# Optimization experiments

Measured on AMD Instinct MI355X. Metric: run time of the kernel, lower is better.

Reference implementation:

```python
import jax, jax.numpy as jnp
import numpy as np

NUM_WIRES = 20
DEPTH = 4


def setup_inputs() -> dict:
    key = jax.random.key(0)
    x = jax.random.normal(key, (NUM_WIRES,), dtype=jnp.float32)
    return {"x": x}


def _apply_1q(state, gate, wire):
    # state: flat [2^n] complex; apply 2x2 gate on `wire`
    s = state.reshape(2 ** wire, 2, -1)
    return jnp.einsum('ab,ibj->iaj', gate, s).reshape(-1)


def _apply_cnot(state, control):
    # CNOT on adjacent wires (control, control+1): flip target where control==1
    s = state.reshape(2 ** control, 2, 2, -1)
    s = jnp.concatenate([s[:, :1], s[:, 1:, ::-1]], axis=1)
    return s.reshape(-1)


def _simulate(x):
    n = NUM_WIRES
    state = jnp.zeros(2 ** n, dtype=jnp.complex64).at[0].set(1.0)
    half = (x.astype(jnp.float32) * 0.5)
    c = jnp.cos(half).astype(jnp.complex64)  # [n]
    s = jnp.sin(half).astype(jnp.complex64)  # [n]
    for _ in range(DEPTH):
        for w in range(n):
            cw, sw = c[w], s[w]
            rx = jnp.stack([jnp.stack([cw, -1j * sw]), jnp.stack([-1j * sw, cw])])
            ry = jnp.stack([jnp.stack([cw, -sw]), jnp.stack([sw, cw])])
            state = _apply_1q(state, rx, w)
            state = _apply_1q(state, ry, w)
        for w in range(n - 1):
            state = _apply_cnot(state, w)
    probs = jnp.abs(state) ** 2  # real float32 [2^n]
    expz = []
    for i in range(n):
        p = probs.reshape(2 ** i, 2, -1).sum(axis=(0, 2))
        expz.append(p[0] - p[1])
    return jnp.stack(expz).astype(jnp.float32)  # [n] <Z_i>


def reference(x):
    return _simulate(x)
```

## Files before the change

### kernel.cpp

```cpp
#include <hip/hip_runtime.h>


#define NW 20

__device__ __forceinline__ float2 cmul(float2 a, float2 b) {
    return make_float2(a.x*b.x - a.y*b.y, a.x*b.y + a.y*b.x);
}

__device__ __forceinline__ void apply_gate(float2& a0, float2& a1,
                                           float2 u00, float2 u01,
                                           float2 u10, float2 u11) {
    float2 b0, b1;
    b0.x = u00.x*a0.x - u00.y*a0.y + u01.x*a1.x - u01.y*a1.y;
    b0.y = u00.x*a0.y + u00.y*a0.x + u01.x*a1.y + u01.y*a1.x;
    b1.x = u10.x*a0.x - u10.y*a0.y + u11.x*a1.x - u11.y*a1.y;
    b1.y = u10.x*a0.y + u10.y*a0.x + u11.x*a1.y + u11.y*a1.x;
    a0 = b0; a1 = b1;
}

__device__ __forceinline__ float2 shflx(float2 v, int m) {
    float2 r;
    r.x = __shfl_xor(v.x, m, 64);
    r.y = __shfl_xor(v.y, m, 64);
    return r;
}

__device__ __forceinline__ unsigned sfx(unsigned x) {
    x ^= x >> 1; x ^= x >> 2; x ^= x >> 4; x ^= x >> 8; x ^= x >> 16; return x;
}

template<int A>
__device__ __forceinline__ void gate_regbit4(float2 (&amp)[4], const float2* Gw) {
    float2 u00 = Gw[0], u01 = Gw[1], u10 = Gw[2], u11 = Gw[3];
    #pragma unroll
    for (int r = 0; r < 4; r++)
        if (!(r & (1 << A)))
            apply_gate(amp[r], amp[r | (1 << A)], u00, u01, u10, u11);
}

template<int A, int LM>
__device__ __forceinline__ void swap_reg_lane4(float2 (&amp)[4], unsigned lane) {
    bool hb = (lane & (unsigned)LM) != 0u;
    #pragma unroll
    for (int r = 0; r < 4; r++) {
        if (!(r & (1 << A))) {
            float2 lo = amp[r], hi = amp[r | (1 << A)];
            float2 xs = hb ? lo : hi;
            float2 ys = shflx(xs, LM);
            amp[r]            = hb ? ys : lo;
            amp[r | (1 << A)] = hb ? hi : ys;
        }
    }
}

__device__ __forceinline__ void prep_Gs(const float* __restrict__ x, float2* Gs,
                                        unsigned t) {
    if (t < NW) {
        float h = 0.5f * x[t];
        float c = cosf(h), s = sinf(h);
        float cc = c*c, ss = s*s, cs = c*s;
        Gs[t*4+0] = make_float2(cc,  ss);
        Gs[t*4+1] = make_float2(-cs, -cs);
        Gs[t*4+2] = make_float2(cs,  -cs);
        Gs[t*4+3] = make_float2(cc,  -ss);
    }
}

template<int MODE>
__global__ __launch_bounds__(1024) void stageA(const float* __restrict__ x,
                                               const float2* __restrict__ src,
                                               float2* __restrict__ dst) {
    __shared__ float2 lds[4096];
    __shared__ float2 Gs[4*NW];
    const unsigned t = threadIdx.x;
    prep_Gs(x, Gs, t);
    __syncthreads();
    const unsigned lane = t & 63u, wv = t >> 6;
    const unsigned w0 = wv & 1u, w1 = (wv >> 1) & 1u, w2 = (wv >> 2) & 1u, w3 = wv >> 3;
    const unsigned H   = blockIdx.x;
    const unsigned Hp  = H ^ (H >> 1);
    const unsigned inj = (H & 1u) << 11;
    const unsigned lb  = (wv << 8) | (lane << 2);
    const unsigned gb  = (lb ^ (lb >> 1)) ^ inj;

    float2 amp[4];
    if (MODE == 1) {
        const float4* q = (const float4*)(src + ((size_t)Hp << 12) + (gb & ~3u));
        float4 q0 = q[0], q1 = q[1];
        float2 e0 = make_float2(q0.x,q0.y), e1 = make_float2(q0.z,q0.w);
        float2 e2 = make_float2(q1.x,q1.y), e3 = make_float2(q1.z,q1.w);
        bool s2 = (gb & 2u) != 0u;
        amp[0] = s2 ? e2 : e0;
        amp[1] = s2 ? e3 : e1;
        amp[2] = s2 ? e1 : e3;
        amp[3] = s2 ? e0 : e2;
    } else {
        float2 P = make_float2(1.0f, 0.0f);
        #pragma unroll
        for (int b = 12; b <= 19; b++)
            P = cmul(P, Gs[(19-b)*4 + (int)((Hp >> (b-12)) & 1u)*2]);
        #pragma unroll
        for (int b = 2; b <= 11; b++)
            P = cmul(P, Gs[(19-b)*4 + (int)((gb >> b) & 1u)*2]);
        float2 T[4];
        #pragma unroll
        for (int j = 0; j < 4; j++)
            T[j] = cmul(P, cmul(Gs[19*4 + (j&1)*2], Gs[18*4 + ((j>>1)&1)*2]));
        bool s2 = (gb & 2u) != 0u;
        amp[0] = s2 ? T[2] : T[0];
        amp[1] = s2 ? T[3] : T[1];
        amp[2] = s2 ? T[1] : T[3];
        amp[3] = s2 ? T[0] : T[2];
    }

    gate_regbit4<0>(amp, Gs + 19*4);
    gate_regbit4<1>(amp, Gs + 18*4);
    swap_reg_lane4<0,1>(amp, lane);
    swap_reg_lane4<1,2>(amp, lane);
    gate_regbit4<0>(amp, Gs + 17*4);
    gate_regbit4<1>(amp, Gs + 16*4);
    swap_reg_lane4<0,4>(amp, lane);
    swap_reg_lane4<1,8>(amp, lane);
    gate_regbit4<0>(amp, Gs + 15*4);
    gate_regbit4<1>(amp, Gs + 14*4);
    swap_reg_lane4<0,16>(amp, lane);
    swap_reg_lane4<1,32>(amp, lane);
    gate_regbit4<0>(amp, Gs + 13*4);
    gate_regbit4<1>(amp, Gs + 12*4);
    #pragma unroll
    for (int k = 0; k < 4; k++) lds[lane | ((unsigned)k << 6) | (wv << 8)] = amp[k];
    __syncthreads();
    #pragma unroll
    for (int k = 0; k < 4; k++)
        amp[k] = lds[lane | (w0 << 6) | (w1 << 7) | ((unsigned)k << 8) | (w2 << 10) | (w3 << 11)];
    gate_regbit4<0>(amp, Gs + 11*4);
    gate_regbit4<1>(amp, Gs + 10*4);
    __syncthreads();
    #pragma unroll
    for (int k = 0; k < 4; k++) lds[lane | ((unsigned)k << 6) | (wv << 8)] = amp[k];
    __syncthreads();
    #pragma unroll
    for (int k = 0; k < 4; k++)
        amp[k] = lds[lane | (w2 << 6) | (w3 << 7) | (w0 << 8) | (w1 << 9) | ((unsigned)k << 10)];
    gate_regbit4<0>(amp, Gs + 9*4);
    gate_regbit4<1>(amp, Gs + 8*4);
    float2* d = dst + ((size_t)H << 12);
    #pragma unroll
    for (int k = 0; k < 4; k++)
        d[lane | (w0 << 6) | (w1 << 7) | (w2 << 8) | (w3 << 9) | ((unsigned)k << 10)] = amp[k];
}

template<int FUSE>
__global__ __launch_bounds__(1024) void stageB(const float* __restrict__ x,
                                               float2* __restrict__ st,
                                               float* __restrict__ partial) {
    __shared__ float2 lds[4096];
    __shared__ float2 Gs[4*NW];
    const unsigned t = threadIdx.x;
    prep_Gs(x, Gs, t);
    __syncthreads();
    const unsigned lane = t & 63u, wv = t >> 6;
    const unsigned w0 = wv & 1u, w1 = (wv >> 1) & 1u, w2 = (wv >> 2) & 1u, w3 = wv >> 3;
    const unsigned bb = blockIdx.x;
    const unsigned m = lane & 15u, l4 = (lane >> 4) & 1u, l5 = lane >> 5;

    float2 amp[4];
    #pragma unroll
    for (int k = 0; k < 4; k++) {
        unsigned h = (unsigned)k | (l4 << 2) | (l5 << 3) | (wv << 4);
        amp[k] = st[((size_t)h << 12) | (bb << 4) | m];
    }
    gate_regbit4<0>(amp, Gs + 7*4);
    gate_regbit4<1>(amp, Gs + 6*4);
    swap_reg_lane4<0,16>(amp, lane);
    swap_reg_lane4<1,32>(amp, lane);
    gate_regbit4<0>(amp, Gs + 5*4);
    gate_regbit4<1>(amp, Gs + 4*4);
    #pragma unroll
    for (int k = 0; k < 4; k++) lds[lane | ((unsigned)k << 6) | (wv << 8)] = amp[k];
    __syncthreads();
    #pragma unroll
    for (int k = 0; k < 4; k++)
        amp[k] = lds[lane | (w0 << 6) | (w1 << 7) | ((unsigned)k << 8) | (w2 << 10) | (w3 << 11)];
    gate_regbit4<0>(amp, Gs + 3*4);
    gate_regbit4<1>(amp, Gs + 2*4);
    __syncthreads();
    #pragma unroll
    for (int k = 0; k < 4; k++) lds[lane | ((unsigned)k << 6) | (wv << 8)] = amp[k];
    __syncthreads();
    #pragma unroll
    for (int k = 0; k < 4; k++)
        amp[k] = lds[lane | (w2 << 6) | (w3 << 7) | (w0 << 8) | (w1 << 9) | ((unsigned)k << 10)];
    gate_regbit4<0>(amp, Gs + 1*4);
    gate_regbit4<1>(amp, Gs + 0*4);

    if (!FUSE) {
        #pragma unroll
        for (int k = 0; k < 4; k++) {
            unsigned h = l4 | (l5 << 1) | (w0 << 2) | (w1 << 3) | (w2 << 4) | (w3 << 5)
                       | (((unsigned)k & 1u) << 6) | (((unsigned)k >> 1) << 7);
            st[((size_t)h << 12) | (bb << 4) | m] = amp[k];
        }
    } else {
        float p[4];
        #pragma unroll
        for (int k = 0; k < 4; k++) p[k] = amp[k].x*amp[k].x + amp[k].y*amp[k].y;
        float S19 = (p[0] + p[1]) - (p[2] + p[3]);
        float D   = p[0] - p[1] - p[2] + p[3];
        unsigned v = m | (bb << 4) | (l4 << 12) | (l5 << 13) | (w0 << 14)
                   | (w1 << 15) | (w2 << 16) | (w3 << 17);
        unsigned cm = sfx(v);
        float acc[NW];
        acc[0] = S19; acc[1] = D;
        #pragma unroll
        for (int w = 2; w < NW; w++)
            acc[w] = ((cm >> (19 - w)) & 1u) ? -D : D;

        __syncthreads();
        float* red = (float*)lds;
        #pragma unroll
        for (int w = 0; w < NW; w++) {
            float s = acc[w];
            #pragma unroll
            for (int off = 32; off; off >>= 1) s += __shfl_down(s, off, 64);
            if (lane == 0) red[wv*NW + w] = s;
        }
        __syncthreads();
        if (t < NW) {
            float s = 0.0f;
            #pragma unroll
            for (int v16 = 0; v16 < 16; v16++) s += red[v16*NW + (int)t];
            partial[bb*NW + t] = s;
        }
    }
}

__global__ __launch_bounds__(256) void reduce_out(const float* __restrict__ partial,
                                                  float* __restrict__ out) {
    __shared__ float red[4*NW];
    unsigned t = threadIdx.x;
    float vals[NW];
    #pragma unroll
    for (int w = 0; w < NW; w++) vals[w] = partial[t*NW + w];
    #pragma unroll
    for (int w = 0; w < NW; w++) {
        float v = vals[w];
        #pragma unroll
        for (int off = 32; off; off >>= 1) v += __shfl_down(v, off, 64);
        if ((t & 63u) == 0u) red[(t >> 6)*NW + w] = v;
    }
    __syncthreads();
    if (t < NW) out[t] = red[t] + red[NW+t] + red[2*NW+t] + red[3*NW+t];
}

extern "C" void kernel_launch(void* const* d_in, const int* in_sizes, int n_in,
                              void* d_out, int out_size, void* d_ws, size_t ws_size,
                              hipStream_t stream) {
    (void)in_sizes; (void)n_in; (void)out_size; (void)ws_size;
    const float* x = (const float*)d_in[0];
    float* out = (float*)d_out;

    char* ws = (char*)d_ws;
    float*  partial = (float*)(ws + 1024);
    float2* buf0    = (float2*)(ws + 65536);
    float2* buf1    = (float2*)(ws + 65536 + (size_t)(8u << 20));

    stageA<0><<<256, 1024, 0, stream>>>(x, buf1 , buf0);
    stageB<0><<<256, 1024, 0, stream>>>(x, buf0, nullptr);
    stageA<1><<<256, 1024, 0, stream>>>(x, buf0, buf1);
    stageB<0><<<256, 1024, 0, stream>>>(x, buf1, nullptr);
    stageA<1><<<256, 1024, 0, stream>>>(x, buf1, buf0);
    stageB<1><<<256, 1024, 0, stream>>>(x, buf0, partial);
    reduce_out<<<1, 256, 0, stream>>>(partial, out);
}
```

Baseline: 63.68 us.

## Fuse layer passes into four kernels with CNOT-parity masked gates

```diff
diff --git a/kernel.cpp b/kernel.cpp
--- a/kernel.cpp
+++ b/kernel.cpp
@@ -25,12 +25,12 @@
     return r;
 }
 
-__device__ __forceinline__ unsigned sfx(unsigned x) {
-    x ^= x >> 1; x ^= x >> 2; x ^= x >> 4; x ^= x >> 8; x ^= x >> 16; return x;
+__device__ __forceinline__ unsigned pfx2(unsigned x) {
+    x ^= x >> 2; x ^= x >> 4; x ^= x >> 8; x ^= x >> 16; return x;
 }
 
 template<int A>
-__device__ __forceinline__ void gate_regbit4(float2 (&amp)[4], const float2* Gw) {
+__device__ __forceinline__ void gate_regbit(float2 (&amp)[4], const float2* Gw) {
     float2 u00 = Gw[0], u01 = Gw[1], u10 = Gw[2], u11 = Gw[3];
     #pragma unroll
     for (int r = 0; r < 4; r++)
@@ -50,6 +50,20 @@
             amp[r]            = hb ? ys : lo;
             amp[r | (1 << A)] = hb ? hi : ys;
         }
+    }
+}
+
+template<int M, int SEL, int RH>
+__device__ __forceinline__ void gate_mreg(float2 (&amp)[4], const float2* Gw,
+                                          unsigned Rk) {
+    float2 u00 = Gw[0], u01 = Gw[1], u10 = Gw[2], u11 = Gw[3];
+    #pragma unroll
+    for (int r = 0; r < 4; r++) {
+        if (r & SEL) continue;
+        int rp = r ^ M;
+        unsigned fl = (Rk + (unsigned)__popc((unsigned)r & (unsigned)RH)) & 1u;
+        if (fl == 0u) apply_gate(amp[r], amp[rp], u00, u01, u10, u11);
+        else          apply_gate(amp[rp], amp[r], u00, u01, u10, u11);
     }
 }
 
@@ -66,9 +80,58 @@
     }
 }
 
-template<int MODE>
-__global__ __launch_bounds__(1024) void stageA(const float* __restrict__ x,
-                                               const float2* __restrict__ src,
+__device__ __forceinline__ void masked_high(float2 (&amp)[4], float2* lds,
+                                            const float2* Gs, unsigned lane,
+                                            unsigned wv) {
+    const unsigned w0 = wv & 1u, w1 = (wv >> 1) & 1u, w2 = (wv >> 2) & 1u, w3 = wv >> 3;
+    const unsigned l3 = (lane >> 3) & 1u, l4 = (lane >> 4) & 1u, l5 = lane >> 5;
+    const unsigned wpar = w0 ^ w1 ^ w2 ^ w3;
+    gate_mreg<3,2,0>(amp, Gs + 0*4, 0u);
+    #pragma unroll
+    for (int k = 0; k < 4; k++) lds[lane | ((unsigned)k << 6) | (wv << 8)] = amp[k];
+    __syncthreads();
+    #pragma unroll
+    for (int k = 0; k < 4; k++)
+        amp[k] = lds[lane | ((unsigned)(k>>1) << 6) | (w3 << 7) | (w0 << 8)
+                     | (w1 << 9) | (w2 << 10) | ((unsigned)(k&1) << 11)];
+    __syncthreads();
+    gate_mreg<3,2,0>(amp, Gs + 1*4, w3);
+    #pragma unroll
+    for (int k = 0; k < 4; k++) lds[lane | ((unsigned)k << 6) | (wv << 8)] = amp[k];
+    __syncthreads();
+    #pragma unroll
+    for (int k = 0; k < 4; k++)
+        amp[k] = lds[lane | ((unsigned)(k>>1) << 6) | (w2 << 7) | (w0 << 8)
+                     | (w1 << 9) | ((unsigned)(k&1) << 10) | (w3 << 11)];
+    __syncthreads();
+    gate_mreg<3,2,0>(amp, Gs + 2*4, w2 ^ w3);
+    #pragma unroll
+    for (int k = 0; k < 4; k++) lds[lane | ((unsigned)k << 6) | (wv << 8)] = amp[k];
+    __syncthreads();
+    #pragma unroll
+    for (int k = 0; k < 4; k++)
+        amp[k] = lds[lane | ((unsigned)(k>>1) << 6) | (w1 << 7) | (w0 << 8)
+                     | ((unsigned)(k&1) << 9) | (w2 << 10) | (w3 << 11)];
+    __syncthreads();
+    gate_mreg<3,2,0>(amp, Gs + 3*4, w1 ^ w2 ^ w3);
+    #pragma unroll
+    for (int k = 0; k < 4; k++) lds[lane | ((unsigned)k << 6) | (wv << 8)] = amp[k];
+    __syncthreads();
+    #pragma unroll
+    for (int k = 0; k < 4; k++)
+        amp[k] = lds[lane | ((unsigned)(k>>1) << 6) | (w0 << 7) | ((unsigned)(k&1) << 8)
+                     | (w1 << 9) | (w2 << 10) | (w3 << 11)];
+    __syncthreads();
+    gate_mreg<3,2,0>(amp, Gs + 4*4, wpar);
+    swap_reg_lane4<1,16>(amp, lane);
+    gate_mreg<3,1,0>(amp, Gs + 5*4, l4 ^ wpar);
+    swap_reg_lane4<0,8>(amp, lane);
+    gate_mreg<3,2,0>(amp, Gs + 6*4, l3 ^ l4 ^ wpar);
+    swap_reg_lane4<1,32>(amp, lane);
+    gate_mreg<3,1,0>(amp, Gs + 7*4, l5 ^ l3 ^ l4 ^ wpar);
+}
+
+__global__ __launch_bounds__(1024) void passA1(const float* __restrict__ x,
                                                float2* __restrict__ dst) {
     __shared__ float2 lds[4096];
     __shared__ float2 Gs[4*NW];
@@ -84,9 +147,139 @@
     const unsigned gb  = (lb ^ (lb >> 1)) ^ inj;
 
     float2 amp[4];
-    if (MODE == 1) {
+    {
+        float2 P = make_float2(1.0f, 0.0f);
+        #pragma unroll
+        for (int b = 12; b <= 19; b++)
+            P = cmul(P, Gs[(19-b)*4 + (int)((Hp >> (b-12)) & 1u)*2]);
+        #pragma unroll
+        for (int b = 2; b <= 11; b++)
+            P = cmul(P, Gs[(19-b)*4 + (int)((gb >> b) & 1u)*2]);
+        float2 T[4];
+        #pragma unroll
+        for (int j = 0; j < 4; j++)
+            T[j] = cmul(P, cmul(Gs[19*4 + (j&1)*2], Gs[18*4 + ((j>>1)&1)*2]));
+        bool s2 = (gb & 2u) != 0u;
+        amp[0] = s2 ? T[2] : T[0];
+        amp[1] = s2 ? T[3] : T[1];
+        amp[2] = s2 ? T[1] : T[3];
+        amp[3] = s2 ? T[0] : T[2];
+    }
+    gate_regbit<0>(amp, Gs + 19*4);
+    gate_regbit<1>(amp, Gs + 18*4);
+    swap_reg_lane4<0,1>(amp, lane);
+    swap_reg_lane4<1,2>(amp, lane);
+    gate_regbit<0>(amp, Gs + 17*4);
+    gate_regbit<1>(amp, Gs + 16*4);
+    swap_reg_lane4<0,4>(amp, lane);
+    swap_reg_lane4<1,8>(amp, lane);
+    gate_regbit<0>(amp, Gs + 15*4);
+    gate_regbit<1>(amp, Gs + 14*4);
+    swap_reg_lane4<0,16>(amp, lane);
+    swap_reg_lane4<1,32>(amp, lane);
+    gate_regbit<0>(amp, Gs + 13*4);
+    gate_regbit<1>(amp, Gs + 12*4);
+    #pragma unroll
+    for (int k = 0; k < 4; k++) lds[lane | ((unsigned)k << 6) | (wv << 8)] = amp[k];
+    __syncthreads();
+    #pragma unroll
+    for (int k = 0; k < 4; k++)
+        amp[k] = lds[lane | (w0 << 6) | (w1 << 7) | ((unsigned)k << 8) | (w2 << 10) | (w3 << 11)];
+    gate_regbit<0>(amp, Gs + 11*4);
+    gate_regbit<1>(amp, Gs + 10*4);
+    __syncthreads();
+    #pragma unroll
+    for (int k = 0; k < 4; k++) lds[lane | ((unsigned)k << 6) | (wv << 8)] = amp[k];
+    __syncthreads();
+    #pragma unroll
+    for (int k = 0; k < 4; k++)
+        amp[k] = lds[lane | (w2 << 6) | (w3 << 7) | (w0 << 8) | (w1 << 9) | ((unsigned)k << 10)];
+    gate_regbit<0>(amp, Gs + 9*4);
+    gate_regbit<1>(amp, Gs + 8*4);
+    float2* d = dst + ((size_t)H << 12);
+    #pragma unroll
+    for (int k = 0; k < 4; k++)
+        d[lane | (w0 << 6) | (w1 << 7) | (w2 << 8) | (w3 << 9) | ((unsigned)k << 10)] = amp[k];
+}
+
+__global__ __launch_bounds__(1024) void passB2(const float* __restrict__ x,
+                                               float2* __restrict__ st) {
+    __shared__ float2 lds[4096];
+    __shared__ float2 Gs[4*NW];
+    const unsigned t = threadIdx.x, lane = t & 63u, wv = t >> 6;
+    const unsigned w0 = wv & 1u, w1 = (wv >> 1) & 1u, w2 = (wv >> 2) & 1u, w3 = wv >> 3;
+    const unsigned bb = blockIdx.x;
+    const unsigned l012 = lane & 7u;
+    const unsigned l3 = (lane >> 3) & 1u, l4 = (lane >> 4) & 1u, l5 = lane >> 5;
+
+    float2 amp[4];
+    const unsigned base = l012 | (bb << 3) | (l5 << 11) | (l3 << 14) | (l4 << 15)
+                        | (w0 << 16) | (w1 << 17) | (w2 << 18) | (w3 << 19);
+    #pragma unroll
+    for (int k = 0; k < 4; k++)
+        amp[k] = st[base | ((unsigned)(k & 1) << 12) | ((unsigned)(k >> 1) << 13)];
+    prep_Gs(x, Gs, t);
+    __syncthreads();
+
+    gate_regbit<0>(amp, Gs + 7*4);
+    gate_regbit<1>(amp, Gs + 6*4);
+    swap_reg_lane4<0,8>(amp, lane);
+    gate_regbit<0>(amp, Gs + 5*4);
+    swap_reg_lane4<1,16>(amp, lane);
+    gate_regbit<1>(amp, Gs + 4*4);
+    #pragma unroll
+    for (int k = 0; k < 4; k++) lds[lane | ((unsigned)k << 6) | (wv << 8)] = amp[k];
+    __syncthreads();
+    #pragma unroll
+    for (int k = 0; k < 4; k++)
+        amp[k] = lds[lane | (w0 << 6) | (w1 << 7) | ((unsigned)(k&1) << 8)
+                     | ((unsigned)(k>>1) << 9) | (w2 << 10) | (w3 << 11)];
+    __syncthreads();
+    gate_regbit<0>(amp, Gs + 3*4);
+    gate_regbit<1>(amp, Gs + 2*4);
+    #pragma unroll
+    for (int k = 0; k < 4; k++) lds[lane | ((unsigned)k << 6) | (wv << 8)] = amp[k];
+    __syncthreads();
+    #pragma unroll
+    for (int k = 0; k < 4; k++)
+        amp[k] = lds[lane | (w2 << 6) | (w3 << 7) | (w0 << 8) | (w1 << 9)
+                     | ((unsigned)(k&1) << 10) | ((unsigned)(k>>1) << 11)];
+    __syncthreads();
+    gate_regbit<0>(amp, Gs + 1*4);
+    gate_regbit<1>(amp, Gs + 0*4);
+
+    masked_high(amp, lds, Gs, lane, wv);
+
+    const unsigned sb = l012 | (bb << 3) | (l5 << 13) | (l3 << 14) | (l4 << 15)
+                      | (w0 << 16) | (w1 << 17) | (w2 << 18) | (w3 << 19);
+    #pragma unroll
+    for (int k = 0; k < 4; k++)
+        st[sb | ((unsigned)(k >> 1) << 11) | ((unsigned)(k & 1) << 12)] = amp[k];
+}
+
+__global__ __launch_bounds__(1024) void passA3(const float* __restrict__ x,
+                                               const float2* __restrict__ src,
+                                               float2* __restrict__ dst) {
+    __shared__ float2 lds[4096];
+    __shared__ float2 Gs[4*NW];
+    const unsigned t = threadIdx.x, lane = t & 63u, wv = t >> 6;
+    const unsigned w0 = wv & 1u, w1 = (wv >> 1) & 1u, w2 = (wv >> 2) & 1u, w3 = wv >> 3;
+    const unsigned H   = blockIdx.x;
+    const unsigned Hp  = H ^ (H >> 1);
+    const unsigned inj = (H & 1u) << 11;
+    const unsigned lb  = (wv << 8) | (lane << 2);
+    const unsigned gb  = (lb ^ (lb >> 1)) ^ inj;
+
+    float4 q0, q1;
+    {
         const float4* q = (const float4*)(src + ((size_t)Hp << 12) + (gb & ~3u));
-        float4 q0 = q[0], q1 = q[1];
+        q0 = q[0]; q1 = q[1];
+    }
+    prep_Gs(x, Gs, t);
+    __syncthreads();
+
+    float2 amp[4];
+    {
         float2 e0 = make_float2(q0.x,q0.y), e1 = make_float2(q0.z,q0.w);
         float2 e2 = make_float2(q1.x,q1.y), e3 = make_float2(q1.z,q1.w);
         bool s2 = (gb & 2u) != 0u;
@@ -94,47 +287,29 @@
         amp[1] = s2 ? e3 : e1;
         amp[2] = s2 ? e1 : e3;
         amp[3] = s2 ? e0 : e2;
-    } else {
-        float2 P = make_float2(1.0f, 0.0f);
-        #pragma unroll
-        for (int b = 12; b <= 19; b++)
-            P = cmul(P, Gs[(19-b)*4 + (int)((Hp >> (b-12)) & 1u)*2]);
-        #pragma unroll
-        for (int b = 2; b <= 11; b++)
-            P = cmul(P, Gs[(19-b)*4 + (int)((gb >> b) & 1u)*2]);
-        float2 T[4];
-        #pragma unroll
-        for (int j = 0; j < 4; j++)
-            T[j] = cmul(P, cmul(Gs[19*4 + (j&1)*2], Gs[18*4 + ((j>>1)&1)*2]));
-        bool s2 = (gb & 2u) != 0u;
-        amp[0] = s2 ? T[2] : T[0];
-        amp[1] = s2 ? T[3] : T[1];
-        amp[2] = s2 ? T[1] : T[3];
-        amp[3] = s2 ? T[0] : T[2];
-    }
-
-    gate_regbit4<0>(amp, Gs + 19*4);
-    gate_regbit4<1>(amp, Gs + 18*4);
+    }
+    gate_regbit<0>(amp, Gs + 19*4);
+    gate_regbit<1>(amp, Gs + 18*4);
     swap_reg_lane4<0,1>(amp, lane);
     swap_reg_lane4<1,2>(amp, lane);
-    gate_regbit4<0>(amp, Gs + 17*4);
-    gate_regbit4<1>(amp, Gs + 16*4);
+    gate_regbit<0>(amp, Gs + 17*4);
+    gate_regbit<1>(amp, Gs + 16*4);
     swap_reg_lane4<0,4>(amp, lane);
     swap_reg_lane4<1,8>(amp, lane);
-    gate_regbit4<0>(amp, Gs + 15*4);
-    gate_regbit4<1>(amp, Gs + 14*4);
+    gate_regbit<0>(amp, Gs + 15*4);
+    gate_regbit<1>(amp, Gs + 14*4);
     swap_reg_lane4<0,16>(amp, lane);
     swap_reg_lane4<1,32>(amp, lane);
-    gate_regbit4<0>(amp, Gs + 13*4);
-    gate_regbit4<1>(amp, Gs + 12*4);
+    gate_regbit<0>(amp, Gs + 13*4);
+    gate_regbit<1>(amp, Gs + 12*4);
     #pragma unroll
     for (int k = 0; k < 4; k++) lds[lane | ((unsigned)k << 6) | (wv << 8)] = amp[k];
     __syncthreads();
     #pragma unroll
     for (int k = 0; k < 4; k++)
         amp[k] = lds[lane | (w0 << 6) | (w1 << 7) | ((unsigned)k << 8) | (w2 << 10) | (w3 << 11)];
-    gate_regbit4<0>(amp, Gs + 11*4);
-    gate_regbit4<1>(amp, Gs + 10*4);
+    gate_regbit<0>(amp, Gs + 11*4);
+    gate_regbit<1>(amp, Gs + 10*4);
     __syncthreads();
     #pragma unroll
     for (int k = 0; k < 4; k++) lds[lane | ((unsigned)k << 6) | (wv << 8)] = amp[k];
@@ -142,96 +317,128 @@
     #pragma unroll
     for (int k = 0; k < 4; k++)
         amp[k] = lds[lane | (w2 << 6) | (w3 << 7) | (w0 << 8) | (w1 << 9) | ((unsigned)k << 10)];
-    gate_regbit4<0>(amp, Gs + 9*4);
-    gate_regbit4<1>(amp, Gs + 8*4);
+    gate_regbit<0>(amp, Gs + 9*4);
+    gate_regbit<1>(amp, Gs + 8*4);
+    __syncthreads();
+
+    const unsigned PH = (unsigned)__popc(H) & 1u;
+    const unsigned wpar = w0 ^ w1 ^ w2 ^ w3;
+    const unsigned lpar = (unsigned)__popc(lane) & 1u;
+    const unsigned l0v = lane & 1u, l1v = (lane >> 1) & 1u;
+    const unsigned l3v = (lane >> 3) & 1u, l4v = (lane >> 4) & 1u, l5v = lane >> 5;
+    swap_reg_lane4<0,1>(amp, lane);
+    swap_reg_lane4<1,2>(amp, lane);
+    gate_mreg<1,1,2>(amp, Gs + 19*4, lpar ^ wpar ^ PH);
+    gate_mreg<3,2,0>(amp, Gs + 18*4, lpar ^ wpar ^ PH);
+    swap_reg_lane4<0,4>(amp, lane);
+    gate_mreg<3,1,0>(amp, Gs + 17*4, l3v^l4v^l5v ^ l0v^l1v ^ wpar ^ PH);
+    swap_reg_lane4<1,8>(amp, lane);
+    gate_mreg<3,2,0>(amp, Gs + 16*4, l4v^l5v ^ l0v^l1v ^ wpar ^ PH);
+    swap_reg_lane4<0,16>(amp, lane);
+    gate_mreg<3,1,0>(amp, Gs + 15*4, l5v ^ l0v^l1v ^ wpar ^ PH);
+    swap_reg_lane4<1,32>(amp, lane);
+    gate_mreg<3,2,0>(amp, Gs + 14*4, l0v^l1v ^ wpar ^ PH);
+    #pragma unroll
+    for (int k = 0; k < 4; k++) lds[lane | ((unsigned)k << 6) | (wv << 8)] = amp[k];
+    __syncthreads();
+    #pragma unroll
+    for (int k = 0; k < 4; k++)
+        amp[k] = lds[lane | (w0 << 6) | ((unsigned)(k&1) << 7) | ((unsigned)(k>>1) << 8)
+                     | (w1 << 9) | (w2 << 10) | (w3 << 11)];
+    __syncthreads();
+    gate_mreg<3,2,0>(amp, Gs + 13*4, w1^w2^w3 ^ l0v^l1v ^ PH);
+    #pragma unroll
+    for (int k = 0; k < 4; k++) lds[lane | ((unsigned)k << 6) | (wv << 8)] = amp[k];
+    __syncthreads();
+    #pragma unroll
+    for (int k = 0; k < 4; k++)
+        amp[k] = lds[lane | (w1 << 6) | ((unsigned)(k&1) << 7) | (w0 << 8)
+                     | ((unsigned)(k>>1) << 9) | (w2 << 10) | (w3 << 11)];
+    __syncthreads();
+    gate_mreg<3,2,0>(amp, Gs + 12*4, w2^w3 ^ l0v^l1v ^ PH);
+    #pragma unroll
+    for (int k = 0; k < 4; k++) lds[lane | ((unsigned)k << 6) | (wv << 8)] = amp[k];
+    __syncthreads();
+    #pragma unroll
+    for (int k = 0; k < 4; k++)
+        amp[k] = lds[lane | (w2 << 6) | ((unsigned)(k&1) << 7) | (w0 << 8)
+                     | (w1 << 9) | ((unsigned)(k>>1) << 10) | (w3 << 11)];
+    __syncthreads();
+    gate_mreg<3,2,0>(amp, Gs + 11*4, w3 ^ l0v^l1v ^ PH);
+    #pragma unroll
+    for (int k = 0; k < 4; k++) lds[lane | ((unsigned)k << 6) | (wv << 8)] = amp[k];
+    __syncthreads();
+    #pragma unroll
+    for (int k = 0; k < 4; k++)
+        amp[k] = lds[lane | (w3 << 6) | ((unsigned)(k&1) << 7) | (w0 << 8)
+                     | (w1 << 9) | (w2 << 10) | ((unsigned)(k>>1) << 11)];
+    gate_mreg<3,2,0>(amp, Gs + 10*4, l0v^l1v ^ PH);
+    swap_reg_lane4<0,1>(amp, lane);
+    gate_mreg<3,1,0>(amp, Gs + 9*4, l1v ^ PH);
+    swap_reg_lane4<1,2>(amp, lane);
+    gate_mreg<3,2,0>(amp, Gs + 8*4, PH);
+    const unsigned sb = ((lane >> 2) & 1u) | (l3v << 1) | (l4v << 2) | (l5v << 3)
+                      | (w0 << 4) | (w1 << 5) | (w2 << 6) | (w3 << 7)
+                      | (l0v << 8) | (l1v << 9);
     float2* d = dst + ((size_t)H << 12);
     #pragma unroll
     for (int k = 0; k < 4; k++)
-        d[lane | (w0 << 6) | (w1 << 7) | (w2 << 8) | (w3 << 9) | ((unsigned)k << 10)] = amp[k];
-}
-
-template<int FUSE>
-__global__ __launch_bounds__(1024) void stageB(const float* __restrict__ x,
-                                               float2* __restrict__ st,
+        d[sb | ((unsigned)(k & 1) << 10) | ((unsigned)(k >> 1) << 11)] = amp[k];
+}
+
+__global__ __launch_bounds__(1024) void passB4(const float* __restrict__ x,
+                                               const float2* __restrict__ st,
                                                float* __restrict__ partial) {
     __shared__ float2 lds[4096];
     __shared__ float2 Gs[4*NW];
-    const unsigned t = threadIdx.x;
-    prep_Gs(x, Gs, t);
-    __syncthreads();
-    const unsigned lane = t & 63u, wv = t >> 6;
+    const unsigned t = threadIdx.x, lane = t & 63u, wv = t >> 6;
     const unsigned w0 = wv & 1u, w1 = (wv >> 1) & 1u, w2 = (wv >> 2) & 1u, w3 = wv >> 3;
     const unsigned bb = blockIdx.x;
-    const unsigned m = lane & 15u, l4 = (lane >> 4) & 1u, l5 = lane >> 5;
+    const unsigned l012 = lane & 7u;
+    const unsigned l3 = (lane >> 3) & 1u, l4 = (lane >> 4) & 1u, l5 = lane >> 5;
 
     float2 amp[4];
-    #pragma unroll
-    for (int k = 0; k < 4; k++) {
-        unsigned h = (unsigned)k | (l4 << 2) | (l5 << 3) | (wv << 4);
-        amp[k] = st[((size_t)h << 12) | (bb << 4) | m];
-    }
-    gate_regbit4<0>(amp, Gs + 7*4);
-    gate_regbit4<1>(amp, Gs + 6*4);
-    swap_reg_lane4<0,16>(amp, lane);
-    swap_reg_lane4<1,32>(amp, lane);
-    gate_regbit4<0>(amp, Gs + 5*4);
-    gate_regbit4<1>(amp, Gs + 4*4);
-    #pragma unroll
-    for (int k = 0; k < 4; k++) lds[lane | ((unsigned)k << 6) | (wv << 8)] = amp[k];
-    __syncthreads();
-    #pragma unroll
-    for (int k = 0; k < 4; k++)
-        amp[k] = lds[lane | (w0 << 6) | (w1 << 7) | ((unsigned)k << 8) | (w2 << 10) | (w3 << 11)];
-    gate_regbit4<0>(amp, Gs + 3*4);
-    gate_regbit4<1>(amp, Gs + 2*4);
-    __syncthreads();
-    #pragma unroll
-    for (int k = 0; k < 4; k++) lds[lane | ((unsigned)k << 6) | (wv << 8)] = amp[k];
-    __syncthreads();
-    #pragma unroll
-    for (int k = 0; k < 4; k++)
-        amp[k] = lds[lane | (w2 << 6) | (w3 << 7) | (w0 << 8) | (w1 << 9) | ((unsigned)k << 10)];
-    gate_regbit4<0>(amp, Gs + 1*4);
-    gate_regbit4<1>(amp, Gs + 0*4);
-
-    if (!FUSE) {
-        #pragma unroll
-        for (int k = 0; k < 4; k++) {
-            unsigned h = l4 | (l5 << 1) | (w0 << 2) | (w1 << 3) | (w2 << 4) | (w3 << 5)
-                       | (((unsigned)k & 1u) << 6) | (((unsigned)k >> 1) << 7);
-            st[((size_t)h << 12) | (bb << 4) | m] = amp[k];
-        }
-    } else {
-        float p[4];
-        #pragma unroll
-        for (int k = 0; k < 4; k++) p[k] = amp[k].x*amp[k].x + amp[k].y*amp[k].y;
-        float S19 = (p[0] + p[1]) - (p[2] + p[3]);
-        float D   = p[0] - p[1] - p[2] + p[3];
-        unsigned v = m | (bb << 4) | (l4 << 12) | (l5 << 13) | (w0 << 14)
-                   | (w1 << 15) | (w2 << 16) | (w3 << 17);
-        unsigned cm = sfx(v);
-        float acc[NW];
-        acc[0] = S19; acc[1] = D;
-        #pragma unroll
-        for (int w = 2; w < NW; w++)
-            acc[w] = ((cm >> (19 - w)) & 1u) ? -D : D;
-
-        __syncthreads();
-        float* red = (float*)lds;
-        #pragma unroll
-        for (int w = 0; w < NW; w++) {
-            float s = acc[w];
-            #pragma unroll
-            for (int off = 32; off; off >>= 1) s += __shfl_down(s, off, 64);
-            if (lane == 0) red[wv*NW + w] = s;
-        }
-        __syncthreads();
-        if (t < NW) {
-            float s = 0.0f;
-            #pragma unroll
-            for (int v16 = 0; v16 < 16; v16++) s += red[v16*NW + (int)t];
-            partial[bb*NW + t] = s;
-        }
+    const unsigned base = l012 | (bb << 3) | (l5 << 11) | (l3 << 12) | (l4 << 13)
+                        | (w0 << 14) | (w1 << 15) | (w2 << 16) | (w3 << 17);
+    #pragma unroll
+    for (int k = 0; k < 4; k++)
+        amp[k] = st[base | ((unsigned)(k & 1) << 18) | ((unsigned)(k >> 1) << 19)];
+    prep_Gs(x, Gs, t);
+    __syncthreads();
+
+    masked_high(amp, lds, Gs, lane, wv);
+
+    float p[4];
+    #pragma unroll
+    for (int k = 0; k < 4; k++) p[k] = amp[k].x*amp[k].x + amp[k].y*amp[k].y;
+    const float T = p[0] + p[1] + p[2] + p[3];
+    const float E = (p[0] + p[2]) - (p[1] + p[3]);
+    const float O = (p[0] + p[1]) - (p[2] + p[3]);
+    const unsigned zbase = l012 | (bb << 3) | (l5 << 13) | (l3 << 14) | (l4 << 15)
+                         | (w0 << 16) | (w1 << 17) | (w2 << 18) | (w3 << 19);
+    const unsigned t2 = pfx2(zbase);
+    float acc[NW];
+    #pragma unroll
+    for (int w = 0; w < NW; w++) {
+        int b = 19 - w;
+        float v = (b >= 13) ? T : ((b & 1) ? O : E);
+        acc[w] = ((t2 >> b) & 1u) ? -v : v;
+    }
+    __syncthreads();
+    float* red = (float*)lds;
+    #pragma unroll
+    for (int w = 0; w < NW; w++) {
+        float s = acc[w];
+        #pragma unroll
+        for (int off = 32; off; off >>= 1) s += __shfl_down(s, off, 64);
+        if (lane == 0) red[wv*NW + w] = s;
+    }
+    __syncthreads();
+    if (t < NW) {
+        float s = 0.0f;
+        #pragma unroll
+        for (int v16 = 0; v16 < 16; v16++) s += red[v16*NW + (int)t];
+        partial[bb*NW + t] = s;
     }
 }
 
@@ -265,11 +472,9 @@
     float2* buf0    = (float2*)(ws + 65536);
     float2* buf1    = (float2*)(ws + 65536 + (size_t)(8u << 20));
 
-    stageA<0><<<256, 1024, 0, stream>>>(x, buf1 , buf0);
-    stageB<0><<<256, 1024, 0, stream>>>(x, buf0, nullptr);
-    stageA<1><<<256, 1024, 0, stream>>>(x, buf0, buf1);
-    stageB<0><<<256, 1024, 0, stream>>>(x, buf1, nullptr);
-    stageA<1><<<256, 1024, 0, stream>>>(x, buf1, buf0);
-    stageB<1><<<256, 1024, 0, stream>>>(x, buf0, partial);
+    passA1<<<256, 1024, 0, stream>>>(x, buf0);
+    passB2<<<256, 1024, 0, stream>>>(x, buf0);
+    passA3<<<256, 1024, 0, stream>>>(x, buf0, buf1);
+    passB4<<<256, 1024, 0, stream>>>(x, buf1, partial);
     reduce_out<<<1, 256, 0, stream>>>(partial, out);
 }
```

New measurement: 80.10 us. 1.26x slower.

## Replace second LDS transpose with lane shuffles and prefetch state before gate prep

Applied to the files above, without the earlier changes.

```diff
diff --git a/kernel.cpp b/kernel.cpp
--- a/kernel.cpp
+++ b/kernel.cpp
@@ -30,7 +30,7 @@
 }
 
 template<int A>
-__device__ __forceinline__ void gate_regbit4(float2 (&amp)[4], const float2* Gw) {
+__device__ __forceinline__ void gate_regbit(float2 (&amp)[4], const float2* Gw) {
     float2 u00 = Gw[0], u01 = Gw[1], u10 = Gw[2], u11 = Gw[3];
     #pragma unroll
     for (int r = 0; r < 4; r++)
@@ -73,20 +73,25 @@
     __shared__ float2 lds[4096];
     __shared__ float2 Gs[4*NW];
     const unsigned t = threadIdx.x;
-    prep_Gs(x, Gs, t);
-    __syncthreads();
     const unsigned lane = t & 63u, wv = t >> 6;
     const unsigned w0 = wv & 1u, w1 = (wv >> 1) & 1u, w2 = (wv >> 2) & 1u, w3 = wv >> 3;
+    const unsigned l4v = (lane >> 4) & 1u, l5v = lane >> 5;
     const unsigned H   = blockIdx.x;
     const unsigned Hp  = H ^ (H >> 1);
     const unsigned inj = (H & 1u) << 11;
     const unsigned lb  = (wv << 8) | (lane << 2);
     const unsigned gb  = (lb ^ (lb >> 1)) ^ inj;
 
+    float4 q0, q1;
+    if (MODE == 1) {
+        const float4* q = (const float4*)(src + ((size_t)Hp << 12) + (gb & ~3u));
+        q0 = q[0]; q1 = q[1];
+    }
+    prep_Gs(x, Gs, t);
+    __syncthreads();
+
     float2 amp[4];
     if (MODE == 1) {
-        const float4* q = (const float4*)(src + ((size_t)Hp << 12) + (gb & ~3u));
-        float4 q0 = q[0], q1 = q[1];
         float2 e0 = make_float2(q0.x,q0.y), e1 = make_float2(q0.z,q0.w);
         float2 e2 = make_float2(q1.x,q1.y), e3 = make_float2(q1.z,q1.w);
         bool s2 = (gb & 2u) != 0u;
@@ -113,41 +118,40 @@
         amp[3] = s2 ? T[0] : T[2];
     }
 
-    gate_regbit4<0>(amp, Gs + 19*4);
-    gate_regbit4<1>(amp, Gs + 18*4);
+    gate_regbit<0>(amp, Gs + 19*4);
+    gate_regbit<1>(amp, Gs + 18*4);
     swap_reg_lane4<0,1>(amp, lane);
     swap_reg_lane4<1,2>(amp, lane);
-    gate_regbit4<0>(amp, Gs + 17*4);
-    gate_regbit4<1>(amp, Gs + 16*4);
+    gate_regbit<0>(amp, Gs + 17*4);
+    gate_regbit<1>(amp, Gs + 16*4);
     swap_reg_lane4<0,4>(amp, lane);
     swap_reg_lane4<1,8>(amp, lane);
-    gate_regbit4<0>(amp, Gs + 15*4);
-    gate_regbit4<1>(amp, Gs + 14*4);
-    swap_reg_lane4<0,16>(amp, lane);
-    swap_reg_lane4<1,32>(amp, lane);
-    gate_regbit4<0>(amp, Gs + 13*4);
-    gate_regbit4<1>(amp, Gs + 12*4);
+    gate_regbit<0>(amp, Gs + 15*4);
+    gate_regbit<1>(amp, Gs + 14*4);
+    swap_reg_lane4<0,16>(amp, lane);
+    swap_reg_lane4<1,32>(amp, lane);
+    gate_regbit<0>(amp, Gs + 13*4);
+    gate_regbit<1>(amp, Gs + 12*4);
     #pragma unroll
     for (int k = 0; k < 4; k++) lds[lane | ((unsigned)k << 6) | (wv << 8)] = amp[k];
     __syncthreads();
     #pragma unroll
     for (int k = 0; k < 4; k++)
-        amp[k] = lds[lane | (w0 << 6) | (w1 << 7) | ((unsigned)k << 8) | (w2 << 10) | (w3 << 11)];
-    gate_regbit4<0>(amp, Gs + 11*4);
-    gate_regbit4<1>(amp, Gs + 10*4);
-    __syncthreads();
-    #pragma unroll
-    for (int k = 0; k < 4; k++) lds[lane | ((unsigned)k << 6) | (wv << 8)] = amp[k];
-    __syncthreads();
-    #pragma unroll
-    for (int k = 0; k < 4; k++)
-        amp[k] = lds[lane | (w2 << 6) | (w3 << 7) | (w0 << 8) | (w1 << 9) | ((unsigned)k << 10)];
-    gate_regbit4<0>(amp, Gs + 9*4);
-    gate_regbit4<1>(amp, Gs + 8*4);
+        amp[k] = lds[(lane & 15u) | (w0 << 4) | (w1 << 5) | (w2 << 6) | (w3 << 7)
+                     | ((unsigned)(k & 1) << 8) | ((unsigned)(k >> 1) << 9)
+                     | (l4v << 10) | (l5v << 11)];
+    gate_regbit<0>(amp, Gs + 11*4);
+    gate_regbit<1>(amp, Gs + 10*4);
+    swap_reg_lane4<0,16>(amp, lane);
+    gate_regbit<0>(amp, Gs + 9*4);
+    swap_reg_lane4<1,32>(amp, lane);
+    gate_regbit<1>(amp, Gs + 8*4);
     float2* d = dst + ((size_t)H << 12);
     #pragma unroll
     for (int k = 0; k < 4; k++)
-        d[lane | (w0 << 6) | (w1 << 7) | (w2 << 8) | (w3 << 9) | ((unsigned)k << 10)] = amp[k];
+        d[(lane & 15u) | (w0 << 4) | (w1 << 5) | (w2 << 6) | (w3 << 7)
+          | (l4v << 8) | (l5v << 9)
+          | ((unsigned)(k & 1) << 10) | ((unsigned)(k >> 1) << 11)] = amp[k];
 }
 
 template<int FUSE>
@@ -157,58 +161,55 @@
     __shared__ float2 lds[4096];
     __shared__ float2 Gs[4*NW];
     const unsigned t = threadIdx.x;
-    prep_Gs(x, Gs, t);
-    __syncthreads();
     const unsigned lane = t & 63u, wv = t >> 6;
     const unsigned w0 = wv & 1u, w1 = (wv >> 1) & 1u, w2 = (wv >> 2) & 1u, w3 = wv >> 3;
+    const unsigned m = lane & 15u, l4v = (lane >> 4) & 1u, l5v = lane >> 5;
     const unsigned bb = blockIdx.x;
-    const unsigned m = lane & 15u, l4 = (lane >> 4) & 1u, l5 = lane >> 5;
 
     float2 amp[4];
-    #pragma unroll
-    for (int k = 0; k < 4; k++) {
-        unsigned h = (unsigned)k | (l4 << 2) | (l5 << 3) | (wv << 4);
-        amp[k] = st[((size_t)h << 12) | (bb << 4) | m];
-    }
-    gate_regbit4<0>(amp, Gs + 7*4);
-    gate_regbit4<1>(amp, Gs + 6*4);
-    swap_reg_lane4<0,16>(amp, lane);
-    swap_reg_lane4<1,32>(amp, lane);
-    gate_regbit4<0>(amp, Gs + 5*4);
-    gate_regbit4<1>(amp, Gs + 4*4);
+    const unsigned lbase = m | (bb << 4) | (l4v << 14) | (l5v << 15)
+                         | (w0 << 16) | (w1 << 17) | (w2 << 18) | (w3 << 19);
+    #pragma unroll
+    for (int k = 0; k < 4; k++)
+        amp[k] = st[lbase | ((unsigned)(k & 1) << 12) | ((unsigned)(k >> 1) << 13)];
+    prep_Gs(x, Gs, t);
+    __syncthreads();
+
+    gate_regbit<0>(amp, Gs + 7*4);
+    gate_regbit<1>(amp, Gs + 6*4);
+    swap_reg_lane4<0,16>(amp, lane);
+    swap_reg_lane4<1,32>(amp, lane);
+    gate_regbit<0>(amp, Gs + 5*4);
+    gate_regbit<1>(amp, Gs + 4*4);
     #pragma unroll
     for (int k = 0; k < 4; k++) lds[lane | ((unsigned)k << 6) | (wv << 8)] = amp[k];
     __syncthreads();
     #pragma unroll
     for (int k = 0; k < 4; k++)
-        amp[k] = lds[lane | (w0 << 6) | (w1 << 7) | ((unsigned)k << 8) | (w2 << 10) | (w3 << 11)];
-    gate_regbit4<0>(amp, Gs + 3*4);
-    gate_regbit4<1>(amp, Gs + 2*4);
-    __syncthreads();
-    #pragma unroll
-    for (int k = 0; k < 4; k++) lds[lane | ((unsigned)k << 6) | (wv << 8)] = amp[k];
-    __syncthreads();
-    #pragma unroll
-    for (int k = 0; k < 4; k++)
-        amp[k] = lds[lane | (w2 << 6) | (w3 << 7) | (w0 << 8) | (w1 << 9) | ((unsigned)k << 10)];
-    gate_regbit4<0>(amp, Gs + 1*4);
-    gate_regbit4<1>(amp, Gs + 0*4);
+        amp[k] = lds[(lane & 15u) | (w0 << 4) | (w1 << 5) | (w2 << 6) | (w3 << 7)
+                     | ((unsigned)(k & 1) << 8) | ((unsigned)(k >> 1) << 9)
+                     | (l4v << 10) | (l5v << 11)];
+    gate_regbit<0>(amp, Gs + 3*4);
+    gate_regbit<1>(amp, Gs + 2*4);
+    swap_reg_lane4<0,16>(amp, lane);
+    gate_regbit<0>(amp, Gs + 1*4);
+    swap_reg_lane4<1,32>(amp, lane);
+    gate_regbit<1>(amp, Gs + 0*4);
 
     if (!FUSE) {
         #pragma unroll
-        for (int k = 0; k < 4; k++) {
-            unsigned h = l4 | (l5 << 1) | (w0 << 2) | (w1 << 3) | (w2 << 4) | (w3 << 5)
-                       | (((unsigned)k & 1u) << 6) | (((unsigned)k >> 1) << 7);
-            st[((size_t)h << 12) | (bb << 4) | m] = amp[k];
-        }
+        for (int k = 0; k < 4; k++)
+            st[m | (bb << 4) | (w0 << 12) | (w1 << 13) | (w2 << 14) | (w3 << 15)
+               | (l4v << 16) | (l5v << 17)
+               | ((unsigned)(k & 1) << 18) | ((unsigned)(k >> 1) << 19)] = amp[k];
     } else {
         float p[4];
         #pragma unroll
         for (int k = 0; k < 4; k++) p[k] = amp[k].x*amp[k].x + amp[k].y*amp[k].y;
         float S19 = (p[0] + p[1]) - (p[2] + p[3]);
         float D   = p[0] - p[1] - p[2] + p[3];
-        unsigned v = m | (bb << 4) | (l4 << 12) | (l5 << 13) | (w0 << 14)
-                   | (w1 << 15) | (w2 << 16) | (w3 << 17);
+        unsigned v = m | (bb << 4) | (w0 << 12) | (w1 << 13) | (w2 << 14)
+                   | (w3 << 15) | (l4v << 16) | (l5v << 17);
         unsigned cm = sfx(v);
         float acc[NW];
         acc[0] = S19; acc[1] = D;
```

Result: slower. 73.37 us (+15.2%).
